# Kernel tuning notes

Hardware: AMD Instinct MI355X
Metric: run time of the kernel (lower is better)

The kernel has to match this reference:

```python
import jax, jax.numpy as jnp
import numpy as np

NEG_SLOPE = 0.2  # LeakyReLU(0.2) on the final Dense


def setup_inputs() -> dict:
    key = jax.random.key(0)
    k1, k2, k3, k4 = jax.random.split(key, 4)
    B, D = 256, 65536          # batch, input voxel dim
    N, G = 41, 2048            # n_groups, group size (overlapping allowed)
    O, E = 256, 512            # per-group output dim, embed_dim
    x = jax.random.normal(k1, (B, D), dtype=jnp.float32)
    group_idx = jax.random.randint(k2, (N, G), 0, D, dtype=jnp.int32)
    # He-normal-ish init for the per-group Dense weights
    W = jax.random.normal(k3, (N, G, O), dtype=jnp.float32) * np.float32(np.sqrt(2.0 / G))
    b = jnp.zeros((N, O), dtype=jnp.float32)
    W3 = jax.random.normal(k4, (N * O, E), dtype=jnp.float32) * np.float32(np.sqrt(2.0 / (N * O)))
    b3 = jnp.zeros((E,), dtype=jnp.float32)
    return {"x": x, "group_idx": group_idx, "W": W, "b": b, "W3": W3, "b3": b3}


def reference(x, group_idx, W, b, W3, b3):
    B = x.shape[0]
    # per-group gather: (B, N, G)
    g = x[:, group_idx]
    # N parallel Dense layers as one grouped GEMM: (B, N, O)
    h = jnp.einsum('bng,ngo->bno', g, W) + b
    # concat along feature axis -> (B, N*O); dropout is identity at inference
    h = h.reshape(B, -1)
    # final Dense + LeakyReLU(0.2)
    out = h @ W3 + b3
    return jnp.where(out >= 0, out, NEG_SLOPE * out)
```

## Files before the change

kernel.cpp:

```cpp
#include <hip/hip_runtime.h>
#include <hip/hip_bf16.h>

#define NB 256
#define DD 65536
#define NN 41
#define GG 2048
#define OO 256
#define NO 10496
#define EE 512
#define NEG_SLOPE 0.2f

typedef __attribute__((ext_vector_type(8))) short bf16x8;
typedef __attribute__((ext_vector_type(4))) float f32x4;
typedef unsigned int u32;

__device__ __forceinline__ void gl_lds16(const __hip_bfloat16* gsrc, __hip_bfloat16* lds) {
    __builtin_amdgcn_global_load_lds((const __attribute__((address_space(1))) u32*)gsrc,
                                     (__attribute__((address_space(3))) u32*)lds, 16, 0, 0);
}

__global__ __launch_bounds__(256) void transpose_cast_k(const float* __restrict__ src,
                                                        __hip_bfloat16* __restrict__ dst,
                                                        int K, int Oc) {
    __shared__ float tile[32][33];
    size_t slab = (size_t)blockIdx.z * K * Oc;
    int k0 = blockIdx.y * 32, o0 = blockIdx.x * 32;
    int tx = threadIdx.x & 31, ty = threadIdx.x >> 5;
    const float* s = src + slab;
#pragma unroll
    for (int i = 0; i < 4; ++i)
        tile[ty + 8 * i][tx] = s[(size_t)(k0 + ty + 8 * i) * Oc + o0 + tx];
    __syncthreads();
    __hip_bfloat16* d = dst + slab;
    int o = threadIdx.x >> 4;
    int kp = threadIdx.x & 15;
#pragma unroll
    for (int i2 = 0; i2 < 2; ++i2) {
        int oo = o + 16 * i2;
        __hip_bfloat162 p;
        p.x = __float2bfloat16(tile[2 * kp][oo]);
        p.y = __float2bfloat16(tile[2 * kp + 1][oo]);
        *(__hip_bfloat162*)&d[(size_t)(o0 + oo) * K + k0 + 2 * kp] = p;
    }
}

__global__ __launch_bounds__(512) void gather_full_k(const float* __restrict__ x,
                                                     const int* __restrict__ idx,
                                                     __hip_bfloat16* __restrict__ g) {
    extern __shared__ __hip_bfloat16 xr[];
    int b = blockIdx.x;
    int t = threadIdx.x;
    const float4* xv = (const float4*)(x + (size_t)b * DD);
#pragma unroll
    for (int i = 0; i < 32; ++i) {
        float4 v = xv[t + 512 * i];
        short4 p;
        p.x = (short)__bfloat16_as_ushort(__float2bfloat16(v.x));
        p.y = (short)__bfloat16_as_ushort(__float2bfloat16(v.y));
        p.z = (short)__bfloat16_as_ushort(__float2bfloat16(v.z));
        p.w = (short)__bfloat16_as_ushort(__float2bfloat16(v.w));
        *(short4*)&xr[(t + 512 * i) * 4] = p;
    }
    __syncthreads();
    const int4* idx4 = (const int4*)idx;
#pragma unroll 1
    for (int n = 0; n < NN; ++n) {
        int4 ii = idx4[n * 512 + t];
        ushort4 o;
        o.x = __bfloat16_as_ushort(xr[ii.x]);
        o.y = __bfloat16_as_ushort(xr[ii.y]);
        o.z = __bfloat16_as_ushort(xr[ii.z]);
        o.w = __bfloat16_as_ushort(xr[ii.w]);
        *(ushort4*)&g[((size_t)n * NB + b) * GG + t * 4] = o;
    }
}

__global__ __launch_bounds__(512) void gather_half_k(const float* __restrict__ x,
                                                     const int* __restrict__ idx,
                                                     __hip_bfloat16* __restrict__ g) {
    __shared__ __align__(16) __hip_bfloat16 xr[32768];
    int b = blockIdx.x >> 1;
    int h = blockIdx.x & 1;
    int t = threadIdx.x;
    const float4* xv = (const float4*)(x + (size_t)b * DD + h * 32768);
#pragma unroll
    for (int i = 0; i < 16; ++i) {
        float4 v = xv[t + 512 * i];
        short4 p;
        p.x = (short)__bfloat16_as_ushort(__float2bfloat16(v.x));
        p.y = (short)__bfloat16_as_ushort(__float2bfloat16(v.y));
        p.z = (short)__bfloat16_as_ushort(__float2bfloat16(v.z));
        p.w = (short)__bfloat16_as_ushort(__float2bfloat16(v.w));
        *(short4*)&xr[(t + 512 * i) * 4] = p;
    }
    __syncthreads();
    const int4* idx4 = (const int4*)idx;
    for (int u = t; u < NN * GG / 4; u += 512) {
        int4 ii = idx4[u];
        int n = u >> 9;
        int k = (u & 511) * 4;
        __hip_bfloat16* dst = &g[((size_t)n * NB + b) * GG + k];
        if ((ii.x >> 15) == h) dst[0] = xr[ii.x & 32767];
        if ((ii.y >> 15) == h) dst[1] = xr[ii.y & 32767];
        if ((ii.z >> 15) == h) dst[2] = xr[ii.z & 32767];
        if ((ii.w >> 15) == h) dst[3] = xr[ii.w & 32767];
    }
}

__global__ __launch_bounds__(512) void gemm1_k(const __hip_bfloat16* __restrict__ g,
                                               const __hip_bfloat16* __restrict__ Wt,
                                               float* __restrict__ part1) {
    int bid = blockIdx.x;
    int n = bid >> 3;
    int s = bid & 1;
    int m0 = ((bid >> 1) & 1) * 128;
    int o0 = ((bid >> 2) & 1) * 128;
    const __hip_bfloat16* srcA = g + ((size_t)n * NB + m0) * GG + s * 1024;
    const __hip_bfloat16* srcB = Wt + ((size_t)n * OO + o0) * GG + s * 1024;
    __shared__ __align__(16) __hip_bfloat16 lA[2][128 * 32];
    __shared__ __align__(16) __hip_bfloat16 lB[2][128 * 32];
    int t = threadIdx.x;
    int lane = t & 63, w = t >> 6;
    int mw = (w >> 2) * 64;
    int ow = (w & 3) * 32;
    int lrow = lane & 15, quad = lane >> 4;
    int r0 = t >> 2, q0 = (t & 3) * 8;
    size_t offA = (size_t)r0 * GG + q0;
    size_t offB = (size_t)r0 * GG + q0;
    f32x4 acc[4][2] = {};

    gl_lds16(srcA + offA, &lA[0][t * 8]);
    gl_lds16(srcB + offB, &lB[0][t * 8]);
    __syncthreads();
#pragma unroll 1
    for (int it = 0; it < 32; ++it) {
        int cur = it & 1;
        if (it + 1 < 32) {
            int k1 = (it + 1) * 32;
            gl_lds16(srcA + offA + k1, &lA[1 - cur][t * 8]);
            gl_lds16(srcB + offB + k1, &lB[1 - cur][t * 8]);
        }
        bf16x8 af[4];
#pragma unroll
        for (int fm = 0; fm < 4; ++fm)
            af[fm] = *(const bf16x8*)&lA[cur][(mw + fm * 16 + lrow) * 32 + quad * 8];
#pragma unroll
        for (int fn = 0; fn < 2; ++fn) {
            bf16x8 bfr = *(const bf16x8*)&lB[cur][(ow + fn * 16 + lrow) * 32 + quad * 8];
#pragma unroll
            for (int fm = 0; fm < 4; ++fm)
                acc[fm][fn] = __builtin_amdgcn_mfma_f32_16x16x32_bf16(af[fm], bfr, acc[fm][fn], 0, 0, 0);
        }
        __syncthreads();
    }
#pragma unroll
    for (int fm = 0; fm < 4; ++fm) {
#pragma unroll
        for (int fn = 0; fn < 2; ++fn) {
            int col = o0 + ow + fn * 16 + lrow;
#pragma unroll
            for (int r = 0; r < 4; ++r) {
                int row = m0 + mw + fm * 16 + quad * 4 + r;
                part1[((size_t)s * NB + row) * NO + n * OO + col] = acc[fm][fn][r];
            }
        }
    }
}

__global__ __launch_bounds__(256) void combine1_k(const float* __restrict__ part1,
                                                  const float* __restrict__ bias,
                                                  __hip_bfloat16* __restrict__ h) {
    int j4 = blockIdx.x * 256 + threadIdx.x;
    const float4* p0 = (const float4*)part1;
    const float4* p1 = p0 + (size_t)NB * NO / 4;
    int jj = j4 % (NO / 4);
    float4 a = p0[j4], c = p1[j4];
    float4 bv = ((const float4*)bias)[jj];
    a.x += c.x + bv.x; a.y += c.y + bv.y; a.z += c.z + bv.z; a.w += c.w + bv.w;
    ushort4 o;
    o.x = __bfloat16_as_ushort(__float2bfloat16(a.x));
    o.y = __bfloat16_as_ushort(__float2bfloat16(a.y));
    o.z = __bfloat16_as_ushort(__float2bfloat16(a.z));
    o.w = __bfloat16_as_ushort(__float2bfloat16(a.w));
    *(ushort4*)&h[(size_t)j4 * 4] = o;
}

__global__ __launch_bounds__(512) void gemm2_k(const __hip_bfloat16* __restrict__ h,
                                               const __hip_bfloat16* __restrict__ W3t,
                                               float* __restrict__ part) {
    int bid = blockIdx.x;
    int s = bid >> 3;
    int m0 = ((bid >> 2) & 1) * 128;
    int e0 = (bid & 3) * 128;
    const __hip_bfloat16* srcA = h + (size_t)m0 * NO + s * 256;
    const __hip_bfloat16* srcB = W3t + (size_t)e0 * NO + s * 256;
    __shared__ __align__(16) __hip_bfloat16 lA[2][128 * 32];
    __shared__ __align__(16) __hip_bfloat16 lB[2][128 * 32];
    int t = threadIdx.x;
    int lane = t & 63, w = t >> 6;
    int mw = (w >> 2) * 64;
    int ew = (w & 3) * 32;
    int lrow = lane & 15, quad = lane >> 4;
    int r0 = t >> 2, q0 = (t & 3) * 8;
    size_t offA = (size_t)r0 * NO + q0;
    size_t offB = (size_t)r0 * NO + q0;
    f32x4 acc[4][2] = {};

    gl_lds16(srcA + offA, &lA[0][t * 8]);
    gl_lds16(srcB + offB, &lB[0][t * 8]);
    __syncthreads();
#pragma unroll 1
    for (int it = 0; it < 8; ++it) {
        int cur = it & 1;
        if (it + 1 < 8) {
            int k1 = (it + 1) * 32;
            gl_lds16(srcA + offA + k1, &lA[1 - cur][t * 8]);
            gl_lds16(srcB + offB + k1, &lB[1 - cur][t * 8]);
        }
        bf16x8 af[4];
#pragma unroll
        for (int fm = 0; fm < 4; ++fm)
            af[fm] = *(const bf16x8*)&lA[cur][(mw + fm * 16 + lrow) * 32 + quad * 8];
#pragma unroll
        for (int fn = 0; fn < 2; ++fn) {
            bf16x8 bfr = *(const bf16x8*)&lB[cur][(ew + fn * 16 + lrow) * 32 + quad * 8];
#pragma unroll
            for (int fm = 0; fm < 4; ++fm)
                acc[fm][fn] = __builtin_amdgcn_mfma_f32_16x16x32_bf16(af[fm], bfr, acc[fm][fn], 0, 0, 0);
        }
        __syncthreads();
    }
#pragma unroll
    for (int fm = 0; fm < 4; ++fm) {
#pragma unroll
        for (int fn = 0; fn < 2; ++fn) {
            int e = e0 + ew + fn * 16 + lrow;
#pragma unroll
            for (int r = 0; r < 4; ++r) {
                int row = m0 + mw + fm * 16 + quad * 4 + r;
                part[((size_t)s * NB + row) * EE + e] = acc[fm][fn][r];
            }
        }
    }
}

__global__ __launch_bounds__(256) void reduce_k(const float* __restrict__ part,
                                                const float* __restrict__ b3,
                                                float* __restrict__ out) {
    int j = blockIdx.x * 256 + threadIdx.x;
    float4 a = make_float4(0.f, 0.f, 0.f, 0.f);
    for (int s = 0; s < NN; ++s) {
        float4 v = ((const float4*)part)[(size_t)s * (NB * EE / 4) + j];
        a.x += v.x; a.y += v.y; a.z += v.z; a.w += v.w;
    }
    float4 bv = ((const float4*)b3)[j & 127];
    a.x += bv.x; a.y += bv.y; a.z += bv.z; a.w += bv.w;
    a.x = a.x >= 0.f ? a.x : NEG_SLOPE * a.x;
    a.y = a.y >= 0.f ? a.y : NEG_SLOPE * a.y;
    a.z = a.z >= 0.f ? a.z : NEG_SLOPE * a.z;
    a.w = a.w >= 0.f ? a.w : NEG_SLOPE * a.w;
    ((float4*)out)[j] = a;
}

extern "C" void kernel_launch(void* const* d_in, const int* in_sizes, int n_in,
                              void* d_out, int out_size, void* d_ws, size_t ws_size,
                              hipStream_t stream) {
    const float* x = (const float*)d_in[0];
    const int* idx = (const int*)d_in[1];
    const float* W = (const float*)d_in[2];
    const float* bias = (const float*)d_in[3];
    const float* W3 = (const float*)d_in[4];
    const float* b3 = (const float*)d_in[5];
    float* out = (float*)d_out;

    char* ws = (char*)d_ws;
    const size_t g_off = 0;
    const size_t g_sz = (size_t)NN * NB * GG * 2;
    const size_t wt_off = g_off + g_sz;
    const size_t wt_sz = (size_t)NN * GG * OO * 2;
    const size_t w3t_off = wt_off + wt_sz;
    const size_t w3t_sz = (size_t)NO * EE * 2;
    const size_t h_off = w3t_off + w3t_sz;
    const size_t h_sz = (size_t)NB * NO * 2;
    const size_t p_off = h_off + h_sz;

    __hip_bfloat16* g = (__hip_bfloat16*)(ws + g_off);
    __hip_bfloat16* Wt = (__hip_bfloat16*)(ws + wt_off);
    __hip_bfloat16* W3t = (__hip_bfloat16*)(ws + w3t_off);
    __hip_bfloat16* h = (__hip_bfloat16*)(ws + h_off);
    float* part1 = (float*)(ws + p_off);
    float* part = (float*)(ws + p_off);

    transpose_cast_k<<<dim3(OO / 32, GG / 32, NN), 256, 0, stream>>>(W, Wt, GG, OO);
    transpose_cast_k<<<dim3(EE / 32, NO / 32, 1), 256, 0, stream>>>(W3, W3t, NO, EE);
    hipError_t aerr = hipFuncSetAttribute(reinterpret_cast<const void*>(gather_full_k),
                                          hipFuncAttributeMaxDynamicSharedMemorySize, 131072);
    if (aerr == hipSuccess) {
        gather_full_k<<<dim3(NB), 512, 131072, stream>>>(x, idx, g);
    } else {
        gather_half_k<<<dim3(512), 512, 0, stream>>>(x, idx, g);
    }
    gemm1_k<<<dim3(328), 512, 0, stream>>>(g, Wt, part1);
    combine1_k<<<dim3(NB * NO / 4 / 256), 256, 0, stream>>>(part1, bias, h);
    gemm2_k<<<dim3(328), 512, 0, stream>>>(h, W3t, part);
    reduce_k<<<dim3(128), 256, 0, stream>>>(part, b3, out);
}
```

Baseline: 276.7 us.

## Retile both GEMMs to 256-thread blocks with four-way split-K and bf16 partials

gemm1 now uses 256-thread blocks, each warp computing a 64x64 sub-tile, and splits K four ways instead of two, giving 656 blocks. Its partial sums are stored as bf16 rather than fp32, which halves the partial-buffer traffic; combine1 sums the four partials. gemm2 is retiled to 128x64 output tiles with 256 threads over 656 blocks. The intent is more blocks in flight and less memory traffic, at the cost of extra precision loss from rounding partials to bf16.

```diff
diff --git a/kernel.cpp b/kernel.cpp
--- a/kernel.cpp
+++ b/kernel.cpp
@@ -107,45 +107,46 @@
     }
 }
 
-__global__ __launch_bounds__(512) void gemm1_k(const __hip_bfloat16* __restrict__ g,
+__global__ __launch_bounds__(256) void gemm1_k(const __hip_bfloat16* __restrict__ g,
                                                const __hip_bfloat16* __restrict__ Wt,
-                                               float* __restrict__ part1) {
+                                               __hip_bfloat16* __restrict__ part1) {
     int bid = blockIdx.x;
-    int n = bid >> 3;
-    int s = bid & 1;
-    int m0 = ((bid >> 1) & 1) * 128;
+    int s = bid & 3;
     int o0 = ((bid >> 2) & 1) * 128;
-    const __hip_bfloat16* srcA = g + ((size_t)n * NB + m0) * GG + s * 1024;
-    const __hip_bfloat16* srcB = Wt + ((size_t)n * OO + o0) * GG + s * 1024;
+    int m0 = ((bid >> 3) & 1) * 128;
+    int n = bid >> 4;
+    const __hip_bfloat16* srcA = g + ((size_t)n * NB + m0) * GG + s * 512;
+    const __hip_bfloat16* srcB = Wt + ((size_t)n * OO + o0) * GG + s * 512;
     __shared__ __align__(16) __hip_bfloat16 lA[2][128 * 32];
     __shared__ __align__(16) __hip_bfloat16 lB[2][128 * 32];
     int t = threadIdx.x;
     int lane = t & 63, w = t >> 6;
-    int mw = (w >> 2) * 64;
-    int ow = (w & 3) * 32;
+    int mw = (w >> 1) * 64, ow = (w & 1) * 64;
     int lrow = lane & 15, quad = lane >> 4;
     int r0 = t >> 2, q0 = (t & 3) * 8;
-    size_t offA = (size_t)r0 * GG + q0;
-    size_t offB = (size_t)r0 * GG + q0;
-    f32x4 acc[4][2] = {};
-
-    gl_lds16(srcA + offA, &lA[0][t * 8]);
-    gl_lds16(srcB + offB, &lB[0][t * 8]);
+    f32x4 acc[4][4] = {};
+
+    gl_lds16(srcA + (size_t)r0 * GG + q0, &lA[0][t * 8]);
+    gl_lds16(srcA + (size_t)(r0 + 64) * GG + q0, &lA[0][(t + 256) * 8]);
+    gl_lds16(srcB + (size_t)r0 * GG + q0, &lB[0][t * 8]);
+    gl_lds16(srcB + (size_t)(r0 + 64) * GG + q0, &lB[0][(t + 256) * 8]);
     __syncthreads();
 #pragma unroll 1
-    for (int it = 0; it < 32; ++it) {
+    for (int it = 0; it < 16; ++it) {
         int cur = it & 1;
-        if (it + 1 < 32) {
+        if (it + 1 < 16) {
             int k1 = (it + 1) * 32;
-            gl_lds16(srcA + offA + k1, &lA[1 - cur][t * 8]);
-            gl_lds16(srcB + offB + k1, &lB[1 - cur][t * 8]);
+            gl_lds16(srcA + (size_t)r0 * GG + k1 + q0, &lA[1 - cur][t * 8]);
+            gl_lds16(srcA + (size_t)(r0 + 64) * GG + k1 + q0, &lA[1 - cur][(t + 256) * 8]);
+            gl_lds16(srcB + (size_t)r0 * GG + k1 + q0, &lB[1 - cur][t * 8]);
+            gl_lds16(srcB + (size_t)(r0 + 64) * GG + k1 + q0, &lB[1 - cur][(t + 256) * 8]);
         }
         bf16x8 af[4];
 #pragma unroll
         for (int fm = 0; fm < 4; ++fm)
             af[fm] = *(const bf16x8*)&lA[cur][(mw + fm * 16 + lrow) * 32 + quad * 8];
 #pragma unroll
-        for (int fn = 0; fn < 2; ++fn) {
+        for (int fn = 0; fn < 4; ++fn) {
             bf16x8 bfr = *(const bf16x8*)&lB[cur][(ow + fn * 16 + lrow) * 32 + quad * 8];
 #pragma unroll
             for (int fm = 0; fm < 4; ++fm)
@@ -156,27 +157,31 @@
 #pragma unroll
     for (int fm = 0; fm < 4; ++fm) {
 #pragma unroll
-        for (int fn = 0; fn < 2; ++fn) {
+        for (int fn = 0; fn < 4; ++fn) {
             int col = o0 + ow + fn * 16 + lrow;
 #pragma unroll
             for (int r = 0; r < 4; ++r) {
                 int row = m0 + mw + fm * 16 + quad * 4 + r;
-                part1[((size_t)s * NB + row) * NO + n * OO + col] = acc[fm][fn][r];
+                part1[((size_t)s * NB + row) * NO + n * OO + col] = __float2bfloat16(acc[fm][fn][r]);
             }
         }
     }
 }
 
-__global__ __launch_bounds__(256) void combine1_k(const float* __restrict__ part1,
+__global__ __launch_bounds__(256) void combine1_k(const __hip_bfloat16* __restrict__ part1,
                                                   const float* __restrict__ bias,
                                                   __hip_bfloat16* __restrict__ h) {
     int j4 = blockIdx.x * 256 + threadIdx.x;
-    const float4* p0 = (const float4*)part1;
-    const float4* p1 = p0 + (size_t)NB * NO / 4;
     int jj = j4 % (NO / 4);
-    float4 a = p0[j4], c = p1[j4];
-    float4 bv = ((const float4*)bias)[jj];
-    a.x += c.x + bv.x; a.y += c.y + bv.y; a.z += c.z + bv.z; a.w += c.w + bv.w;
+    float4 a = ((const float4*)bias)[jj];
+#pragma unroll
+    for (int s = 0; s < 4; ++s) {
+        ushort4 p = *(const ushort4*)&part1[(size_t)s * NB * NO + (size_t)j4 * 4];
+        a.x += __bfloat162float(__ushort_as_bfloat16(p.x));
+        a.y += __bfloat162float(__ushort_as_bfloat16(p.y));
+        a.z += __bfloat162float(__ushort_as_bfloat16(p.z));
+        a.w += __bfloat162float(__ushort_as_bfloat16(p.w));
+    }
     ushort4 o;
     o.x = __bfloat16_as_ushort(__float2bfloat16(a.x));
     o.y = __bfloat16_as_ushort(__float2bfloat16(a.y));
@@ -185,37 +190,37 @@
     *(ushort4*)&h[(size_t)j4 * 4] = o;
 }
 
-__global__ __launch_bounds__(512) void gemm2_k(const __hip_bfloat16* __restrict__ h,
+__global__ __launch_bounds__(256) void gemm2_k(const __hip_bfloat16* __restrict__ h,
                                                const __hip_bfloat16* __restrict__ W3t,
                                                float* __restrict__ part) {
     int bid = blockIdx.x;
-    int s = bid >> 3;
-    int m0 = ((bid >> 2) & 1) * 128;
-    int e0 = (bid & 3) * 128;
+    int e0 = (bid & 7) * 64;
+    int m0 = ((bid >> 3) & 1) * 128;
+    int s = bid >> 4;
     const __hip_bfloat16* srcA = h + (size_t)m0 * NO + s * 256;
     const __hip_bfloat16* srcB = W3t + (size_t)e0 * NO + s * 256;
     __shared__ __align__(16) __hip_bfloat16 lA[2][128 * 32];
-    __shared__ __align__(16) __hip_bfloat16 lB[2][128 * 32];
+    __shared__ __align__(16) __hip_bfloat16 lB[2][64 * 32];
     int t = threadIdx.x;
     int lane = t & 63, w = t >> 6;
-    int mw = (w >> 2) * 64;
-    int ew = (w & 3) * 32;
+    int mw = (w >> 1) * 64, ew = (w & 1) * 32;
     int lrow = lane & 15, quad = lane >> 4;
-    int r0 = t >> 2, q0 = (t & 3) * 8;
-    size_t offA = (size_t)r0 * NO + q0;
-    size_t offB = (size_t)r0 * NO + q0;
+    int rA = t >> 2, qA = (t & 3) * 8;
+    int rB = t >> 2, qB = (t & 3) * 8;
     f32x4 acc[4][2] = {};
 
-    gl_lds16(srcA + offA, &lA[0][t * 8]);
-    gl_lds16(srcB + offB, &lB[0][t * 8]);
+    gl_lds16(srcA + (size_t)rA * NO + qA, &lA[0][t * 8]);
+    gl_lds16(srcA + (size_t)(rA + 64) * NO + qA, &lA[0][(t + 256) * 8]);
+    gl_lds16(srcB + (size_t)(rB & 63) * NO + qB, &lB[0][t * 8]);
     __syncthreads();
 #pragma unroll 1
     for (int it = 0; it < 8; ++it) {
         int cur = it & 1;
         if (it + 1 < 8) {
             int k1 = (it + 1) * 32;
-            gl_lds16(srcA + offA + k1, &lA[1 - cur][t * 8]);
-            gl_lds16(srcB + offB + k1, &lB[1 - cur][t * 8]);
+            gl_lds16(srcA + (size_t)rA * NO + k1 + qA, &lA[1 - cur][t * 8]);
+            gl_lds16(srcA + (size_t)(rA + 64) * NO + k1 + qA, &lA[1 - cur][(t + 256) * 8]);
+            gl_lds16(srcB + (size_t)(rB & 63) * NO + k1 + qB, &lB[1 - cur][t * 8]);
         }
         bf16x8 af[4];
 #pragma unroll
@@ -288,7 +293,7 @@
     __hip_bfloat16* Wt = (__hip_bfloat16*)(ws + wt_off);
     __hip_bfloat16* W3t = (__hip_bfloat16*)(ws + w3t_off);
     __hip_bfloat16* h = (__hip_bfloat16*)(ws + h_off);
-    float* part1 = (float*)(ws + p_off);
+    __hip_bfloat16* part1 = (__hip_bfloat16*)(ws + p_off);
     float* part = (float*)(ws + p_off);
 
     transpose_cast_k<<<dim3(OO / 32, GG / 32, NN), 256, 0, stream>>>(W, Wt, GG, OO);
@@ -300,8 +305,8 @@
     } else {
         gather_half_k<<<dim3(512), 512, 0, stream>>>(x, idx, g);
     }
-    gemm1_k<<<dim3(328), 512, 0, stream>>>(g, Wt, part1);
+    gemm1_k<<<dim3(656), 256, 0, stream>>>(g, Wt, part1);
     combine1_k<<<dim3(NB * NO / 4 / 256), 256, 0, stream>>>(part1, bias, h);
-    gemm2_k<<<dim3(328), 512, 0, stream>>>(h, W3t, part);
+    gemm2_k<<<dim3(656), 256, 0, stream>>>(h, W3t, part);
     reduce_k<<<dim3(128), 256, 0, stream>>>(part, b3, out);
 }
```

Measured after the change: 275.3 us. About the same (-0.5%).
